# Kernel tuning notes

Hardware: AMD Instinct MI355X
Metric: run time of the kernel (lower is better)

The kernel has to match this reference:

```python
import jax, jax.numpy as jnp
import numpy as np

# Dimensions
B, V, K, H = 64, 2048, 128, 128   # graphs, verts/graph, eigenvectors, h_dim
N = B * V                          # total verts
E = 1048576                        # total neighbor entries
CF = 47                            # chem feat dim = 15 + 2*num_gdf (num_gdf=16)
L = 3                              # num_prop_layers
EPS = 1e-5                         # BatchNorm eps
PROP_SCALE = 1.0                   # propagation_time_scale


def setup_inputs() -> dict:
    key = jax.random.key(0)
    ks = iter(jax.random.split(key, 48))
    nk = lambda: next(ks)
    nrm = lambda shape, s: jax.random.normal(nk(), shape, jnp.float32) * s

    chem_feats = jax.random.normal(nk(), (E, CF), jnp.float32)
    nbr_vid = jax.random.randint(nk(), (E,), 0, N)
    # eigs layout per graph: row 0 = eigen_vals (K,), rows 1..V = eigen_vecs (V,K),
    # rows V+1..2V = eigen_vecs_inv stored as (V,K) (transposed at use site)
    eig_vals = jax.random.uniform(nk(), (B, 1, K), jnp.float32) * 2.0
    vecs = jax.random.normal(nk(), (B, V, K), jnp.float32) / np.sqrt(V)
    vecs_inv = jax.random.normal(nk(), (B, V, K), jnp.float32) / np.sqrt(V)
    eigs = jnp.concatenate([eig_vals, vecs, vecs_inv], axis=1)  # [B, 1+2V, K]

    inp = dict(chem_feats=chem_feats, nbr_vid=nbr_vid, eigs=eigs)
    # chem_mlp params
    inp.update(w1=nrm((CF, H), 0.1), b1=jnp.zeros(H), g1=jnp.ones(H), be1=jnp.zeros(H),
               w2=nrm((H, 2 * H), 0.1), b2=jnp.zeros(2 * H), g2=jnp.ones(2 * H), be2=jnp.zeros(2 * H))
    # propagation layers (stacked across L)
    inp.update(prop_time=jnp.abs(jax.random.normal(nk(), (L, H), jnp.float32)) + 0.1,
               pw1=nrm((L, 2 * H, H), 0.05), pb1=jnp.zeros((L, H)), pg1=jnp.ones((L, H)), pbe1=jnp.zeros((L, H)),
               pw2=nrm((L, H, H), 0.05), pb2=jnp.zeros((L, H)), pg2=jnp.ones((L, H)), pbe2=jnp.zeros((L, H)))
    # out_mlp params
    inp.update(wo1=nrm((H, H), 0.1), bo1=jnp.zeros(H), go1=jnp.ones(H), beo1=jnp.zeros(H),
               wo2=nrm((H, 1), 0.1), bo2=jnp.zeros(1))
    return inp


def _bn(x, g, b):
    # BatchNorm1d in training mode: biased batch stats
    m = jnp.mean(x, axis=0)
    v = jnp.var(x, axis=0)
    return g * (x - m) * jax.lax.rsqrt(v + EPS) + b


def reference(chem_feats, nbr_vid, eigs, w1, b1, g1, be1, w2, b2, g2, be2,
              prop_time, pw1, pb1, pg1, pbe1, pw2, pb2, pg2, pbe2,
              wo1, bo1, go1, beo1, wo2, bo2):
    # --- FeatExtractor ---
    h_chem = _bn(chem_feats @ w1 + b1, g1, be1)
    h_chem = jax.nn.silu(h_chem)
    h_chem = _bn(h_chem @ w2 + b2, g2, be2)             # [E, 2H]
    nbr_filter, nbr_core = h_chem[:, :H], h_chem[:, H:]
    msg = jax.nn.sigmoid(nbr_filter) * jax.nn.softplus(nbr_core)
    h = jax.ops.segment_sum(msg, nbr_vid, num_segments=N)  # [N, H]

    # --- eigen decomposition pieces (uniform per-graph sizes -> batched) ---
    eigen_vals = eigs[:, 0, :]                      # [B, K]
    evecs = eigs[:, 1:1 + V, :]                     # [B, V, K]
    evecs_inv = jnp.swapaxes(eigs[:, 1 + V:, :], 1, 2)  # [B, K, V]

    # --- PropagationLayers ---
    for l in range(L):
        pt = prop_time[l]
        # torch clamps .data in-place under no_grad, then uses it: value clamped, grad passes
        pt = pt + jax.lax.stop_gradient(jnp.clip(pt, 1e-6) - pt)
        time = PROP_SCALE * pt                      # [H]
        hb = h.reshape(B, V, H)
        h_spec = jnp.einsum('bkv,bvh->bkh', evecs_inv, hb)
        coeff = jnp.exp(-eigen_vals[:, :, None] * time[None, None, :])  # [B, K, H]
        h_prop = jnp.einsum('bvk,bkh->bvh', evecs, coeff * h_spec).reshape(N, H)
        z = jnp.concatenate([h, h_prop], axis=-1)   # [N, 2H]
        z = jax.nn.silu(_bn(z @ pw1[l] + pb1[l], pg1[l], pbe1[l]))
        z = _bn(z @ pw2[l] + pb2[l], pg2[l], pbe2[l])
        h = h + z

    # --- out_mlp + per-graph mean ---
    out = jax.nn.silu(_bn(h @ wo1 + bo1, go1, beo1)) @ wo2 + bo2  # [N, 1]
    return out.reshape(B, V, 1).mean(axis=1)        # [B, 1]
```

## Files before the change

### kernel.cpp

```cpp
#include <hip/hip_runtime.h>
#include <hip/hip_bf16.h>
#include <math.h>

#define E_N 1048576
#define CF 47
#define H 128
#define H2 256
#define B_N 64
#define V_N 2048
#define K_N 128
#define N_N 131072
#define EPSf 1e-5f
#define EVS 132

typedef __attribute__((ext_vector_type(8))) short short8;
typedef __attribute__((ext_vector_type(4))) float f32x4;

__device__ __forceinline__ float bf2f(unsigned int u16) {
  union { float f; unsigned int i; } x; x.i = u16 << 16; return x.f;
}
__device__ __forceinline__ unsigned int f2bf_rne(float f) {
  unsigned int u = __float_as_uint(f);
  return (u + 0x7fffu + ((u >> 16) & 1u)) >> 16;
}
__device__ __forceinline__ unsigned int packbf2(float lo, float hi) {
  return f2bf_rne(lo) | (f2bf_rne(hi) << 16);
}
__device__ __forceinline__ float frcp_(float x) { return __builtin_amdgcn_rcpf(x); }
__device__ __forceinline__ float sigmf_(float x) { return frcp_(1.f + __expf(-x)); }
__device__ __forceinline__ float siluf_(float x) { return x * sigmf_(x); }
__device__ __forceinline__ float splusf_(float x) {
  return (x > 15.f) ? x : __logf(1.f + __expf(x));
}

extern "C" __global__ void k_packB1(const float* __restrict__ w1, __hip_bfloat16* __restrict__ B1)
{
  const int i = blockIdx.x * 256 + threadIdx.x;
  const int j = i & 7, L = (i >> 3) & 63, s = (i >> 9) & 1, t = i >> 10;
  const int k = s * 32 + ((L >> 4) * 8) + j;
  const int n = t * 16 + (L & 15);
  B1[i] = __float2bfloat16((k < CF) ? w1[k * H + n] : 0.f);
}

extern "C" __global__ __launch_bounds__(256) void k_gemm1_stats(
    const float* __restrict__ chem, const __hip_bfloat16* __restrict__ B1,
    const float* __restrict__ b1, __hip_bfloat16* __restrict__ x1,
    float* __restrict__ sum1, float* __restrict__ ssq1)
{
  __shared__ __align__(16) unsigned short As[128 * 136];
  __shared__ float bsh[128], cs[128], cq[128];
  float* Afp = (float*)As;
  const int tid = threadIdx.x;
  const int w = tid >> 6, L = tid & 63, lm = L & 15, q = L >> 4;
  const int m0 = w * 32;
  const size_t rowbase = (size_t)blockIdx.x * 128;
  if (tid < 128) { bsh[tid] = b1[tid]; cs[tid] = 0.f; cq[tid] = 0.f; }
  for (int i = tid * 4; i < 128 * CF; i += 1024)
    *(float4*)&Afp[i] = *(const float4*)&chem[rowbase * CF + i];
  __syncthreads();

  short8 fa[2][2];
  #pragma unroll
  for (int mi = 0; mi < 2; ++mi) {
    const int row = m0 + mi * 16 + lm;
    #pragma unroll
    for (int s = 0; s < 2; ++s) {
      union { unsigned int u[4]; short8 s8; } cvt;
      #pragma unroll
      for (int jp = 0; jp < 4; ++jp) {
        const int k0i = s * 32 + q * 8 + jp * 2;
        const float lo = (k0i     < CF) ? Afp[row * CF + k0i]     : 0.f;
        const float hi = (k0i + 1 < CF) ? Afp[row * CF + k0i + 1] : 0.f;
        cvt.u[jp] = packbf2(lo, hi);
      }
      fa[mi][s] = cvt.s8;
    }
  }
  __syncthreads();

  f32x4 acc[2][8];
  #pragma unroll
  for (int mi = 0; mi < 2; ++mi)
    #pragma unroll
    for (int t = 0; t < 8; ++t) acc[mi][t] = (f32x4){0.f, 0.f, 0.f, 0.f};
  const short8* bp = (const short8*)B1;
  #pragma unroll
  for (int s = 0; s < 2; ++s)
    #pragma unroll
    for (int t = 0; t < 8; ++t) {
      const short8 bf = bp[(t * 2 + s) * 64 + L];
      acc[0][t] = __builtin_amdgcn_mfma_f32_16x16x32_bf16(fa[0][s], bf, acc[0][t], 0, 0, 0);
      acc[1][t] = __builtin_amdgcn_mfma_f32_16x16x32_bf16(fa[1][s], bf, acc[1][t], 0, 0, 0);
    }

  float cs8[8], cq8[8];
  #pragma unroll
  for (int t = 0; t < 8; ++t) { cs8[t] = 0.f; cq8[t] = 0.f; }
  #pragma unroll
  for (int t = 0; t < 8; ++t) {
    const int c = t * 16 + lm;
    const float bb = bsh[c];
    #pragma unroll
    for (int mi = 0; mi < 2; ++mi)
      #pragma unroll
      for (int r = 0; r < 4; ++r) {
        const float v = acc[mi][t][r] + bb;
        cs8[t] += v; cq8[t] += v * v;
        As[(m0 + mi * 16 + q * 4 + r) * 136 + c] = (unsigned short)f2bf_rne(v);
      }
  }
  #pragma unroll
  for (int t = 0; t < 8; ++t) {
    cs8[t] += __shfl_xor(cs8[t], 16); cs8[t] += __shfl_xor(cs8[t], 32);
    cq8[t] += __shfl_xor(cq8[t], 16); cq8[t] += __shfl_xor(cq8[t], 32);
  }
  if (q == 0) {
    #pragma unroll
    for (int t = 0; t < 8; ++t) {
      atomicAdd(&cs[t * 16 + lm], cs8[t]);
      atomicAdd(&cq[t * 16 + lm], cq8[t]);
    }
  }
  __syncthreads();
  for (int i = tid; i < 128 * 16; i += 256) {
    const int r = i >> 4, cc = (i & 15) * 8;
    *(uint4*)(x1 + (rowbase + r) * H + cc) = *(const uint4*)&As[r * 136 + cc];
  }
  if (tid < 128) {
    atomicAdd(&sum1[tid], cs[tid]);
    atomicAdd(&ssq1[tid], cq[tid]);
  }
}

extern "C" __global__ void k_bnfin(const float* __restrict__ sum, const float* __restrict__ ssq,
    const float* __restrict__ g, const float* __restrict__ be, float invn,
    float* __restrict__ sc, float* __restrict__ sh)
{
  const int c = threadIdx.x;
  const float m = sum[c] * invn;
  const float v = ssq[c] * invn - m * m;
  const float s = g[c] * rsqrtf(v + EPSf);
  sc[c] = s;
  sh[c] = be[c] - m * s;
}

extern "C" __global__ __launch_bounds__(256) void k_a1_gram(
    __hip_bfloat16* __restrict__ x1, const float* __restrict__ sc1,
    const float* __restrict__ sh1, float* __restrict__ asum, float* __restrict__ G)
{
  __shared__ __align__(16) unsigned short frag[2][16384];
  const int tid = threadIdx.x;
  const int rb = tid >> 4, u = tid & 15;
  const int kb = rb >> 2, qw = rb & 3;
  const int th = u >> 1;
  const int cmb = (u & 1) * 8;
  const int cg = u * 8;
  const int w = tid >> 6;
  const int lq = (tid >> 4) & 3;
  const int cm = tid & 15;
  const int tib = (w >> 1) * 4, tjb = (w & 1) * 4;

  float scv[8], shv[8];
  #pragma unroll
  for (int jc = 0; jc < 8; ++jc) { scv[jc] = sc1[cg + jc]; shv[jc] = sh1[cg + jc]; }

  float cs8[8] = {0.f, 0.f, 0.f, 0.f, 0.f, 0.f, 0.f, 0.f};
  f32x4 acc[4][4];
  #pragma unroll
  for (int a = 0; a < 4; ++a)
    #pragma unroll
    for (int b = 0; b < 4; ++b) acc[a][b] = (f32x4){0.f, 0.f, 0.f, 0.f};

  const int ldsbase = kb * 4096 + th * 512 + qw * 128;
  uint4 rv[8];

  auto PROCESS = [&](int bsel, size_t tb) {
    unsigned int colw[8][4];
    #pragma unroll
    for (int jc = 0; jc < 8; ++jc) { colw[jc][0] = 0; colw[jc][1] = 0; colw[jc][2] = 0; colw[jc][3] = 0; }
    #pragma unroll
    for (int j8 = 0; j8 < 8; ++j8) {
      const uint4 pk = rv[j8];
      float f[8];
      f[0] = bf2f(pk.x & 0xffff); f[1] = bf2f(pk.x >> 16);
      f[2] = bf2f(pk.y & 0xffff); f[3] = bf2f(pk.y >> 16);
      f[4] = bf2f(pk.z & 0xffff); f[5] = bf2f(pk.z >> 16);
      f[6] = bf2f(pk.w & 0xffff); f[7] = bf2f(pk.w >> 16);
      unsigned int bfv[8];
      #pragma unroll
      for (int jc = 0; jc < 8; ++jc) {
        f[jc] = siluf_(f[jc] * scv[jc] + shv[jc]);
        cs8[jc] += f[jc];
        bfv[jc] = f2bf_rne(f[jc]);
        colw[jc][j8 >> 1] |= bfv[jc] << (16 * (j8 & 1));
      }
      uint4 o;
      o.x = bfv[0] | (bfv[1] << 16); o.y = bfv[2] | (bfv[3] << 16);
      o.z = bfv[4] | (bfv[5] << 16); o.w = bfv[6] | (bfv[7] << 16);
      *(uint4*)(x1 + (tb + (size_t)(rb * 8 + j8)) * H + cg) = o;
    }
    #pragma unroll
    for (int jc = 0; jc < 8; ++jc) {
      const int pos = (cmb + jc + 2 * th) & 15;
      uint4 cw;
      cw.x = colw[jc][0]; cw.y = colw[jc][1]; cw.z = colw[jc][2]; cw.w = colw[jc][3];
      *(uint4*)&frag[bsel][ldsbase + pos * 8] = cw;
    }
  };

  {
    const size_t tb = (size_t)blockIdx.x * 128;
    #pragma unroll
    for (int j8 = 0; j8 < 8; ++j8)
      rv[j8] = *(const uint4*)(x1 + (tb + (size_t)(rb * 8 + j8)) * H + cg);
    PROCESS(0, tb);
  }

  for (int k = 0; k < 16; ++k) {
    __syncthreads();
    const int cur = k & 1;
    const bool hasnext = (k + 1 < 16);
    const size_t tbn = (size_t)(blockIdx.x + (k + 1) * 512) * 128;
    if (hasnext) {
      #pragma unroll
      for (int j8 = 0; j8 < 8; ++j8)
        rv[j8] = *(const uint4*)(x1 + (tbn + (size_t)(rb * 8 + j8)) * H + cg);
    }
    #pragma unroll
    for (int kk = 0; kk < 4; ++kk) {
      short8 fa[4], fb[4];
      #pragma unroll
      for (int a = 0; a < 4; ++a) {
        const int T = tib + a;
        fa[a] = *(const short8*)&frag[cur][kk * 4096 + T * 512 + lq * 128 + ((cm + 2 * T) & 15) * 8];
      }
      #pragma unroll
      for (int b = 0; b < 4; ++b) {
        const int T = tjb + b;
        fb[b] = *(const short8*)&frag[cur][kk * 4096 + T * 512 + lq * 128 + ((cm + 2 * T) & 15) * 8];
      }
      #pragma unroll
      for (int a = 0; a < 4; ++a)
        #pragma unroll
        for (int b = 0; b < 4; ++b)
          acc[a][b] = __builtin_amdgcn_mfma_f32_16x16x32_bf16(fa[a], fb[b], acc[a][b], 0, 0, 0);
    }
    if (hasnext) PROCESS(cur ^ 1, tbn);
  }

  #pragma unroll
  for (int jc = 0; jc < 8; ++jc) {
    cs8[jc] += __shfl_xor(cs8[jc], 16);
    cs8[jc] += __shfl_xor(cs8[jc], 32);
  }
  __syncthreads();
  float* redp = (float*)&frag[0][0];
  if ((tid & 63) < 16) {
    #pragma unroll
    for (int jc = 0; jc < 8; ++jc) redp[w * 128 + (tid & 15) * 8 + jc] = cs8[jc];
  }
  __syncthreads();
  if (tid < 128)
    atomicAdd(&asum[tid], redp[tid] + redp[128 + tid] + redp[256 + tid] + redp[384 + tid]);

  #pragma unroll
  for (int a = 0; a < 4; ++a)
    #pragma unroll
    for (int b = 0; b < 4; ++b)
      #pragma unroll
      for (int r = 0; r < 4; ++r)
        atomicAdd(&G[((tib + a) * 16 + lq * 4 + r) * 128 + (tjb + b) * 16 + cm], acc[a][b][r]);
}

extern "C" __global__ __launch_bounds__(256) void k_bn2fin(
    const float* __restrict__ asum, const float* __restrict__ Gm,
    const float* __restrict__ w2, const float* __restrict__ g2,
    const float* __restrict__ be2, float* __restrict__ sc2, float* __restrict__ sh2)
{
  __shared__ float Gs[128 * 128];
  __shared__ float w2s[128 * 128];
  __shared__ float mus[128];
  __shared__ float red[512];
  const int tid = threadIdx.x;
  const int jbase = blockIdx.x * 128;
  for (int i = tid; i < 128 * 128; i += 256) {
    Gs[i] = Gm[i];
    w2s[i] = w2[(i >> 7) * H2 + jbase + (i & 127)];
  }
  if (tid < 128) mus[tid] = asum[tid] * (1.f / (float)E_N);
  __syncthreads();
  const int jj = tid & 127, ih = tid >> 7;
  float m1 = 0.f, q = 0.f;
  for (int i = ih * 64; i < ih * 64 + 64; ++i) {
    const float wi = w2s[i * 128 + jj];
    m1 += mus[i] * wi;
    float si = 0.f;
    #pragma unroll 4
    for (int k = 0; k < 128; ++k) si += Gs[i * 128 + k] * w2s[k * 128 + jj];
    q += wi * si;
  }
  red[tid] = m1; red[256 + tid] = q;
  __syncthreads();
  if (ih == 0) {
    const float m1t = red[jj] + red[jj + 128];
    const float qt  = red[256 + jj] + red[256 + jj + 128];
    const float var = qt * (1.f / (float)E_N) - m1t * m1t;
    const float s = g2[jbase + jj] * rsqrtf(var + EPSf);
    sc2[jbase + jj] = s;
    sh2[jbase + jj] = be2[jbase + jj] - m1t * s;
  }
}

extern "C" __global__ __launch_bounds__(256) void k_hist(
    const int* __restrict__ nbr, int* __restrict__ cnt)
{
  const int e = blockIdx.x * 256 + threadIdx.x;
  atomicAdd(&cnt[nbr[e]], 1);
}

extern "C" __global__ __launch_bounds__(256) void k_scan1(
    const int* __restrict__ cnt, int* __restrict__ bsum)
{
  __shared__ int rs[256];
  const int tid = threadIdx.x, b = blockIdx.x;
  const int4 c = *(const int4*)&cnt[b * 1024 + tid * 4];
  rs[tid] = c.x + c.y + c.z + c.w;
  __syncthreads();
  for (int o = 128; o > 0; o >>= 1) {
    if (tid < o) rs[tid] += rs[tid + o];
    __syncthreads();
  }
  if (tid == 0) bsum[b] = rs[0];
}

extern "C" __global__ void k_scan2(const int* __restrict__ bsum, int* __restrict__ bpre)
{
  __shared__ int bs[128];
  const int tid = threadIdx.x;
  bs[tid] = bsum[tid];
  __syncthreads();
  int p = 0;
  for (int i = 0; i < tid; ++i) p += bs[i];
  bpre[tid] = p;
}

extern "C" __global__ __launch_bounds__(256) void k_scan3(
    const int* __restrict__ cnt, const int* __restrict__ bpre,
    int* __restrict__ cursor, int* __restrict__ rowptr)
{
  __shared__ int tsum[256];
  const int tid = threadIdx.x, b = blockIdx.x;
  const int4 c = *(const int4*)&cnt[b * 1024 + tid * 4];
  const int t1 = c.x, t2 = c.x + c.y, t3 = c.x + c.y + c.z, tot = t3 + c.w;
  tsum[tid] = tot;
  __syncthreads();
  for (int o = 1; o < 256; o <<= 1) {
    const int add = (tid >= o) ? tsum[tid - o] : 0;
    __syncthreads();
    tsum[tid] += add;
    __syncthreads();
  }
  const int excl = (tid == 0) ? 0 : tsum[tid - 1];
  const int base = bpre[b] + excl;
  int4 o4;
  o4.x = base; o4.y = base + t1; o4.z = base + t2; o4.w = base + t3;
  *(int4*)&cursor[b * 1024 + tid * 4] = o4;
  *(int4*)&rowptr[b * 1024 + tid * 4] = o4;
}

extern "C" __global__ __launch_bounds__(256) void k_scatteridx(
    const int* __restrict__ nbr, int* __restrict__ cursor,
    int* __restrict__ sorted_eid)
{
  const int e = blockIdx.x * 256 + threadIdx.x;
  const int v = nbr[e];
  const int pos = atomicAdd(&cursor[v], 1);
  sorted_eid[pos] = e;
}

extern "C" __global__ void k_packB(const float* __restrict__ w2, __hip_bfloat16* __restrict__ Bpack)
{
  const int i = blockIdx.x * 256 + threadIdx.x;
  const int j = i & 7, L = (i >> 3) & 63, s = (i >> 9) & 3, t = i >> 11;
  const int k = s * 32 + (L >> 4) * 8 + j;
  const int n = t * 16 + (L & 15);
  Bpack[i] = __float2bfloat16(w2[k * H2 + n]);
}

extern "C" __global__ __launch_bounds__(256) void k_msg(
    const __hip_bfloat16* __restrict__ a1, const int* __restrict__ sorted_eid,
    const __hip_bfloat16* __restrict__ Bpack,
    const float* __restrict__ sc2, const float* __restrict__ sh2,
    __hip_bfloat16* __restrict__ msgbuf, const int eoff)
{
  __shared__ __hip_bfloat16 As[128 * 136];
  __shared__ int eidsh[128];
  __shared__ float sc2s[256], sh2s[256];
  const int tid = threadIdx.x;
  const int s0 = blockIdx.x * 128;
  if (tid < 128) eidsh[tid] = sorted_eid[eoff + s0 + tid];
  sc2s[tid] = sc2[tid]; sh2s[tid] = sh2[tid];
  __syncthreads();
  for (int i = tid; i < 128 * 16; i += 256) {
    const int r = i >> 4, cc = (i & 15) * 8;
    *(uint4*)&As[r * 136 + cc] = *(const uint4*)(a1 + (size_t)eidsh[r] * H + cc);
  }
  __syncthreads();
  const int w = tid >> 6, L = tid & 63, lm = L & 15, q = L >> 4;
  const int m0 = w * 32, m1 = w * 32 + 16;
  f32x4 acc0[16], acc1[16];
  #pragma unroll
  for (int t = 0; t < 16; ++t) { acc0[t] = (f32x4){0.f,0.f,0.f,0.f}; acc1[t] = (f32x4){0.f,0.f,0.f,0.f}; }
  const short8* bp = (const short8*)Bpack;
  #pragma unroll
  for (int s = 0; s < 4; ++s) {
    const short8 af0 = *(const short8*)&As[(m0 + lm) * 136 + s * 32 + q * 8];
    const short8 af1 = *(const short8*)&As[(m1 + lm) * 136 + s * 32 + q * 8];
    #pragma unroll
    for (int t = 0; t < 16; ++t) {
      const short8 bf = bp[(t * 4 + s) * 64 + L];
      acc0[t] = __builtin_amdgcn_mfma_f32_16x16x32_bf16(af0, bf, acc0[t], 0, 0, 0);
      acc1[t] = __builtin_amdgcn_mfma_f32_16x16x32_bf16(af1, bf, acc1[t], 0, 0, 0);
    }
  }
  #pragma unroll
  for (int t = 0; t < 8; ++t) {
    const int cF = t * 16 + lm;
    const float scF = sc2s[cF], shF = sh2s[cF];
    const float scC = sc2s[128 + cF], shC = sh2s[128 + cF];
    #pragma unroll
    for (int r = 0; r < 4; ++r) {
      const int row0 = m0 + q * 4 + r, row1 = m1 + q * 4 + r;
      const float f0 = acc0[t][r] * scF + shF;
      const float g0 = acc0[t + 8][r] * scC + shC;
      const float f1 = acc1[t][r] * scF + shF;
      const float g1 = acc1[t + 8][r] * scC + shC;
      ((unsigned short*)As)[row0 * 136 + cF] = (unsigned short)f2bf_rne(sigmf_(f0) * splusf_(g0));
      ((unsigned short*)As)[row1 * 136 + cF] = (unsigned short)f2bf_rne(sigmf_(f1) * splusf_(g1));
    }
  }
  __syncthreads();
  for (int i = tid; i < 128 * 16; i += 256) {
    const int r = i >> 4, cc = (i & 15) * 8;
    *(uint4*)(msgbuf + ((size_t)(s0 + r)) * H + cc) = *(const uint4*)&As[r * 136 + cc];
  }
}

extern "C" __global__ __launch_bounds__(256) void k_segsum(
    const __hip_bfloat16* __restrict__ msgbuf, const int* __restrict__ rowptr,
    const int* __restrict__ cnt, float* __restrict__ h,
    const int w0, const int w1, const int mode)
{
  __shared__ float redA[256], redB[256];
  const int tid = threadIdx.x;
  const int c2 = (tid & 63) * 2;
  const int j  = tid >> 6;
  const int n0 = blockIdx.x * 16;
  for (int g = 0; g < 16; ++g) {
    const int n = n0 + g;
    const int s = rowptr[n], e = s + cnt[n];
    const int lo = max(s, w0), hi = min(e, w1);
    float s0 = 0.f, s1 = 0.f;
    for (int r = lo + j; r < hi; r += 4) {
      const unsigned int pk = *(const unsigned int*)(msgbuf + ((size_t)(r - w0)) * H + c2);
      s0 += bf2f(pk & 0xffff);
      s1 += bf2f(pk >> 16);
    }
    redA[tid] = s0; redB[tid] = s1;
    __syncthreads();
    if (j == 0) {
      const int t = tid;
      const float t0 = redA[t] + redA[t + 64] + redA[t + 128] + redA[t + 192];
      const float t1 = redB[t] + redB[t + 64] + redB[t + 128] + redB[t + 192];
      float* hp = h + (size_t)n * H + c2;
      if (mode == 0) { hp[0] = t0; hp[1] = t1; }
      else           { hp[0] += t0; hp[1] += t1; }
    }
    __syncthreads();
  }
}

extern "C" __global__ __launch_bounds__(256) void k_spec(
    const float* __restrict__ eigs, const float* __restrict__ h,
    const float* __restrict__ prop_time, int l, float* __restrict__ CS)
{
  __shared__ float Ash[64 * 32];
  __shared__ float Hsh[64 * 128];
  const int tid = threadIdx.x;
  const int b = blockIdx.x >> 2;
  const int kbase = (blockIdx.x & 3) * 32;
  const int k0 = (tid >> 5) * 4;
  const int c0 = (tid & 31) * 4;
  const size_t ebase = (size_t)b * (4097 * 128);
  float acc[4][4] = {};
  for (int vb = 0; vb < V_N; vb += 64) {
    __syncthreads();
    for (int i = tid * 4; i < 64 * 32; i += 1024) {
      const int vv = i >> 5, kk = i & 31;
      *(float4*)&Ash[i] = *(const float4*)&eigs[ebase + (size_t)(2049 + vb + vv) * 128 + kbase + kk];
    }
    for (int i = tid * 4; i < 64 * 128; i += 1024)
      *(float4*)&Hsh[i] = *(const float4*)&h[((size_t)b * V_N + vb) * 128 + i];
    __syncthreads();
    for (int vv = 0; vv < 64; ++vv) {
      const float4 av = *(const float4*)&Ash[vv * 32 + k0];
      const float4 hv = *(const float4*)&Hsh[vv * 128 + c0];
      const float aa[4] = {av.x, av.y, av.z, av.w};
      const float hh[4] = {hv.x, hv.y, hv.z, hv.w};
      #pragma unroll
      for (int a = 0; a < 4; ++a)
        #pragma unroll
        for (int j = 0; j < 4; ++j) acc[a][j] += aa[a] * hh[j];
    }
  }
  #pragma unroll
  for (int a = 0; a < 4; ++a) {
    const float ev = eigs[ebase + kbase + k0 + a];
    #pragma unroll
    for (int j = 0; j < 4; ++j) {
      const float tm = fmaxf(prop_time[l * H + c0 + j], 1e-6f);
      CS[((size_t)b * K_N + kbase + k0 + a) * H + c0 + j] = __expf(-ev * tm) * acc[a][j];
    }
  }
}

extern "C" __global__ __launch_bounds__(256) void k_hprop(
    const float* __restrict__ eigs, const float* __restrict__ CS,
    float* __restrict__ hprop)
{
  __shared__ float EvT[32 * EVS];
  __shared__ float CSsh[32 * 128];
  const int tid = threadIdx.x;
  const int b = blockIdx.x >> 4;
  const int vbase = (blockIdx.x & 15) * 128;
  const int v0 = (tid >> 4) * 8;
  const int c0 = (tid & 15) * 8;
  const size_t ebase = (size_t)b * (4097 * 128);
  float acc[8][8] = {};
  for (int kb = 0; kb < K_N; kb += 32) {
    __syncthreads();
    for (int i = tid; i < 128 * 32; i += 256) {
      const int vv = i >> 5, kk = i & 31;
      EvT[kk * EVS + vv] = eigs[ebase + (size_t)(1 + vbase + vv) * 128 + kb + kk];
    }
    for (int i = tid * 4; i < 32 * 128; i += 1024)
      *(float4*)&CSsh[i] = *(const float4*)&CS[((size_t)b * K_N + kb) * 128 + i];
    __syncthreads();
    for (int kk = 0; kk < 32; ++kk) {
      const float4 ea = *(const float4*)&EvT[kk * EVS + v0];
      const float4 eb = *(const float4*)&EvT[kk * EVS + v0 + 4];
      const float4 ca = *(const float4*)&CSsh[kk * 128 + c0];
      const float4 cb = *(const float4*)&CSsh[kk * 128 + c0 + 4];
      const float ee[8] = {ea.x, ea.y, ea.z, ea.w, eb.x, eb.y, eb.z, eb.w};
      const float cc[8] = {ca.x, ca.y, ca.z, ca.w, cb.x, cb.y, cb.z, cb.w};
      #pragma unroll
      for (int a = 0; a < 8; ++a)
        #pragma unroll
        for (int j = 0; j < 8; ++j) acc[a][j] += ee[a] * cc[j];
    }
  }
  #pragma unroll
  for (int a = 0; a < 8; ++a) {
    const size_t row = ((size_t)b * V_N + vbase + v0 + a) * H;
    #pragma unroll
    for (int j = 0; j < 8; j += 4) {
      float4 o;
      o.x = acc[a][j]; o.y = acc[a][j+1]; o.z = acc[a][j+2]; o.w = acc[a][j+3];
      *(float4*)&hprop[row + c0 + j] = o;
    }
  }
}

extern "C" __global__ __launch_bounds__(256) void k_gemm(
    const float* __restrict__ A0, const float* __restrict__ A1,
    const float* __restrict__ W, const float* __restrict__ bias,
    const float* __restrict__ preSc, const float* __restrict__ preSh,
    const int preop, const int KcA, float* __restrict__ out,
    float* __restrict__ sum, float* __restrict__ ssq)
{
  __shared__ float AT[32 * EVS];
  __shared__ float Ws[32 * 128];
  __shared__ float cs[128], cq[128];
  const int tid = threadIdx.x;
  const int rbase = blockIdx.x * 128;
  const int r0 = (tid >> 4) * 8;
  const int c0 = (tid & 15) * 8;
  float acc[8][8] = {};
  for (int kb = 0; kb < KcA; kb += 32) {
    const float* Asrc = (kb < 128) ? A0 : A1;
    const int kloc = kb & 127;
    __syncthreads();
    for (int i = tid; i < 128 * 32; i += 256) {
      const int rr = i >> 5, kk = i & 31;
      float v = Asrc[((size_t)rbase + rr) * H + kloc + kk];
      if (preop) {
        v = v * preSc[kloc + kk] + preSh[kloc + kk];
        v = siluf_(v);
      }
      AT[kk * EVS + rr] = v;
    }
    for (int i = tid * 4; i < 32 * 128; i += 1024)
      *(float4*)&Ws[i] = *(const float4*)&W[(size_t)kb * 128 + i];
    __syncthreads();
    for (int kk = 0; kk < 32; ++kk) {
      const float4 aa4 = *(const float4*)&AT[kk * EVS + r0];
      const float4 ab4 = *(const float4*)&AT[kk * EVS + r0 + 4];
      const float4 wa4 = *(const float4*)&Ws[kk * 128 + c0];
      const float4 wb4 = *(const float4*)&Ws[kk * 128 + c0 + 4];
      const float ar[8] = {aa4.x, aa4.y, aa4.z, aa4.w, ab4.x, ab4.y, ab4.z, ab4.w};
      const float wr[8] = {wa4.x, wa4.y, wa4.z, wa4.w, wb4.x, wb4.y, wb4.z, wb4.w};
      #pragma unroll
      for (int a = 0; a < 8; ++a)
        #pragma unroll
        for (int j = 0; j < 8; ++j) acc[a][j] += ar[a] * wr[j];
    }
  }
  if (tid < 128) { cs[tid] = 0.f; cq[tid] = 0.f; }
  __syncthreads();
  float s8[8] = {}, q8[8] = {};
  #pragma unroll
  for (int a = 0; a < 8; ++a) {
    const size_t row = ((size_t)rbase + r0 + a) * H;
    float val[8];
    #pragma unroll
    for (int j = 0; j < 8; ++j) {
      val[j] = acc[a][j] + bias[c0 + j];
      s8[j] += val[j];
      q8[j] += val[j] * val[j];
    }
    #pragma unroll
    for (int j = 0; j < 8; j += 4) {
      float4 o; o.x = val[j]; o.y = val[j+1]; o.z = val[j+2]; o.w = val[j+3];
      *(float4*)&out[row + c0 + j] = o;
    }
  }
  #pragma unroll
  for (int j = 0; j < 8; ++j) {
    atomicAdd(&cs[c0 + j], s8[j]);
    atomicAdd(&cq[c0 + j], q8[j]);
  }
  __syncthreads();
  if (tid < 128) {
    atomicAdd(&sum[tid], cs[tid]);
    atomicAdd(&ssq[tid], cq[tid]);
  }
}

extern "C" __global__ __launch_bounds__(256) void k_hupd(
    float* __restrict__ h, const float* __restrict__ tb,
    const float* __restrict__ sc, const float* __restrict__ sh)
{
  const int i4 = blockIdx.x * 256 + threadIdx.x;
  const size_t base = (size_t)i4 * 4;
  const int c = (int)(base & 127);
  float4 t = *(const float4*)&tb[base];
  float4 hh = *(const float4*)&h[base];
  hh.x += sc[c+0]*t.x + sh[c+0];
  hh.y += sc[c+1]*t.y + sh[c+1];
  hh.z += sc[c+2]*t.z + sh[c+2];
  hh.w += sc[c+3]*t.w + sh[c+3];
  *(float4*)&h[base] = hh;
}

extern "C" __global__ __launch_bounds__(256) void k_head(
    const float* __restrict__ ta, const float* __restrict__ sc,
    const float* __restrict__ sh, const float* __restrict__ wo2,
    const float* __restrict__ bo2, float* __restrict__ out)
{
  __shared__ float w2s[128], scs[128], shs[128];
  __shared__ float wred[4];
  const int tid = threadIdx.x;
  if (tid < 128) { w2s[tid] = wo2[tid]; scs[tid] = sc[tid]; shs[tid] = sh[tid]; }
  __syncthreads();
  const int b = blockIdx.x;
  const int wave = tid >> 6, lane = tid & 63;
  const int j = lane * 2;
  const float w0 = w2s[j], w1 = w2s[j+1];
  const float s0 = scs[j], s1 = scs[j+1], t0 = shs[j], t1 = shs[j+1];
  float p = 0.f;
  for (int v = wave; v < V_N; v += 4) {
    const float2 xv = *(const float2*)&ta[((size_t)b * V_N + v) * H + j];
    float x0 = xv.x * s0 + t0; x0 = siluf_(x0);
    float x1 = xv.y * s1 + t1; x1 = siluf_(x1);
    p += x0 * w0 + x1 * w1;
  }
  #pragma unroll
  for (int off = 32; off > 0; off >>= 1) p += __shfl_down(p, off);
  if (lane == 0) wred[wave] = p;
  __syncthreads();
  if (tid == 0) out[b] = (wred[0] + wred[1] + wred[2] + wred[3]) * (1.f / V_N) + bo2[0];
}

extern "C" void kernel_launch(void* const* d_in, const int* in_sizes, int n_in,
                              void* d_out, int out_size, void* d_ws, size_t ws_size,
                              hipStream_t stream) {
  (void)in_sizes; (void)n_in; (void)out_size;
  const float* chem = (const float*)d_in[0];
  const int*   nbr  = (const int*)d_in[1];
  const float* eigs = (const float*)d_in[2];
  const float* w1   = (const float*)d_in[3];
  const float* b1   = (const float*)d_in[4];
  const float* g1   = (const float*)d_in[5];
  const float* be1  = (const float*)d_in[6];
  const float* w2   = (const float*)d_in[7];
  const float* b2   = (const float*)d_in[8];  (void)b2;
  const float* g2   = (const float*)d_in[9];
  const float* be2  = (const float*)d_in[10];
  const float* prop_time = (const float*)d_in[11];
  const float* pw1  = (const float*)d_in[12];
  const float* pb1  = (const float*)d_in[13];
  const float* pg1  = (const float*)d_in[14];
  const float* pbe1 = (const float*)d_in[15];
  const float* pw2  = (const float*)d_in[16];
  const float* pb2  = (const float*)d_in[17];
  const float* pg2  = (const float*)d_in[18];
  const float* pbe2 = (const float*)d_in[19];
  const float* wo1  = (const float*)d_in[20];
  const float* bo1  = (const float*)d_in[21];
  const float* go1  = (const float*)d_in[22];
  const float* beo1 = (const float*)d_in[23];
  const float* wo2  = (const float*)d_in[24];
  const float* bo2  = (const float*)d_in[25];

  float* ws = (float*)d_ws;
  float* h     = ws;
  float* hprop = h + (size_t)N_N * H;
  float* ta    = hprop + (size_t)N_N * H;
  float* CS    = ta + (size_t)N_N * H;
  float* acc   = CS + (size_t)B_N * K_N * H;
  float* sum1 = acc,        *ssq1 = acc + 128;
  float* sc1  = acc + 256,  *sh1  = acc + 384;
  float* asum = acc + 512;
  float* G    = acc + 640;
  float* sc2  = acc + 17024, *sh2 = acc + 17280;
  float* statS = acc + 17536;
  float* scA = acc + 19456, *shA = acc + 19584;
  float* scB = acc + 19712, *shB = acc + 19840;
  __hip_bfloat16* x1 = (__hip_bfloat16*)(acc + 19968);

  char* p = (char*)x1 + (size_t)E_N * H * 2;
  int* cnt        = (int*)p;  p += (size_t)N_N * 4;
  int* cursor     = (int*)p;  p += (size_t)N_N * 4;
  int* rowptr     = (int*)p;  p += (size_t)N_N * 4;
  int* bsum       = (int*)p;  p += 512;
  int* bpre       = (int*)p;  p += 512;
  int* sorted_eid = (int*)p;  p += (size_t)E_N * 4;
  __hip_bfloat16* Bpack = (__hip_bfloat16*)p;  p += 65536;
  __hip_bfloat16* B1pack = (__hip_bfloat16*)p; p += 16384;

  const size_t req = (size_t)(p - (char*)d_ws);
  if (ws_size < req) return;

  __hip_bfloat16* msgbuf = (__hip_bfloat16*)hprop;

  hipMemsetAsync(acc, 0, 19456 * sizeof(float), stream);
  hipMemsetAsync(cnt, 0, (size_t)N_N * sizeof(int), stream);

  k_packB1<<<32, 256, 0, stream>>>(w1, B1pack);
  k_gemm1_stats<<<E_N / 128, 256, 0, stream>>>(chem, B1pack, b1, x1, sum1, ssq1);
  k_bnfin<<<1, 128, 0, stream>>>(sum1, ssq1, g1, be1, 1.f / (float)E_N, sc1, sh1);
  k_a1_gram<<<512, 256, 0, stream>>>(x1, sc1, sh1, asum, G);
  k_bn2fin<<<2, 256, 0, stream>>>(asum, G, w2, g2, be2, sc2, sh2);

  k_packB<<<128, 256, 0, stream>>>(w2, Bpack);
  k_hist<<<E_N / 256, 256, 0, stream>>>(nbr, cnt);
  k_scan1<<<128, 256, 0, stream>>>(cnt, bsum);
  k_scan2<<<1, 128, 0, stream>>>(bsum, bpre);
  k_scan3<<<128, 256, 0, stream>>>(cnt, bpre, cursor, rowptr);
  k_scatteridx<<<E_N / 256, 256, 0, stream>>>(nbr, cursor, sorted_eid);

  for (int half = 0; half < 2; ++half) {
    const int w0 = half * (E_N / 2), w1e = w0 + E_N / 2;
    k_msg<<<(E_N / 2) / 128, 256, 0, stream>>>(x1, sorted_eid, Bpack, sc2, sh2, msgbuf, w0);
    k_segsum<<<N_N / 16, 256, 0, stream>>>(msgbuf, rowptr, cnt, h, w0, w1e, half);
  }

  float* tb = hprop;
  for (int l = 0; l < 3; ++l) {
    k_spec<<<B_N * 4, 256, 0, stream>>>(eigs, h, prop_time, l, CS);
    k_hprop<<<B_N * 16, 256, 0, stream>>>(eigs, CS, hprop);
    k_gemm<<<N_N / 128, 256, 0, stream>>>(h, hprop, pw1 + (size_t)l * H2 * H, pb1 + l * H,
                                          nullptr, nullptr, 0, H2, ta,
                                          statS + (2 * l) * 256, statS + (2 * l) * 256 + 128);
    k_bnfin<<<1, 128, 0, stream>>>(statS + (2 * l) * 256, statS + (2 * l) * 256 + 128,
                                   pg1 + l * H, pbe1 + l * H, 1.f / (float)N_N, scA, shA);
    k_gemm<<<N_N / 128, 256, 0, stream>>>(ta, nullptr, pw2 + (size_t)l * H * H, pb2 + l * H,
                                          scA, shA, 1, H, tb,
                                          statS + (2 * l + 1) * 256, statS + (2 * l + 1) * 256 + 128);
    k_bnfin<<<1, 128, 0, stream>>>(statS + (2 * l + 1) * 256, statS + (2 * l + 1) * 256 + 128,
                                   pg2 + l * H, pbe2 + l * H, 1.f / (float)N_N, scB, shB);
    k_hupd<<<N_N * H / 1024, 256, 0, stream>>>(h, tb, scB, shB);
  }

  k_gemm<<<N_N / 128, 256, 0, stream>>>(h, nullptr, wo1, bo1, nullptr, nullptr, 0, H, ta,
                                        statS + 6 * 256, statS + 6 * 256 + 128);
  k_bnfin<<<1, 128, 0, stream>>>(statS + 6 * 256, statS + 6 * 256 + 128,
                                 go1, beo1, 1.f / (float)N_N, scA, shA);
  k_head<<<B_N, 256, 0, stream>>>(ta, scA, shA, wo2, bo2, (float*)d_out);
}
```

Baseline: 3.258 ms.

## Move propagation and output GEMMs to split-bf16 MFMA with prepacked weights

Replaces the scalar FP32 tiled GEMM, used for the propagation MLPs and the output MLP, with an MFMA kernel. It splits both activations and weights into bf16 hi/lo parts and accumulates three bf16 products to approximate FP32 accuracy. Weights are prepacked into the MFMA operand layout by a new pack kernel, and the BN statistics reduction is redone using wave shuffles. The goal is to cut the FP32 FMA compute cost of seven N×128 GEMMs, at the price of three times the MFMA work and a small loss of precision.

```diff
diff --git a/kernel.cpp b/kernel.cpp
--- a/kernel.cpp
+++ b/kernel.cpp
@@ -40,6 +40,20 @@
   const int k = s * 32 + ((L >> 4) * 8) + j;
   const int n = t * 16 + (L & 15);
   B1[i] = __float2bfloat16((k < CF) ? w1[k * H + n] : 0.f);
+}
+
+extern "C" __global__ void k_packW(const float* __restrict__ W,
+    __hip_bfloat16* __restrict__ hi, __hip_bfloat16* __restrict__ lo, const int NS)
+{
+  const int i = blockIdx.x * 256 + threadIdx.x;
+  const int j = i & 7, L = (i >> 3) & 63, ts = i >> 9;
+  const int s = ts % NS, t = ts / NS;
+  const int k = s * 32 + (L >> 4) * 8 + j;
+  const int n = t * 16 + (L & 15);
+  const float w = W[k * H + n];
+  const unsigned int h16 = f2bf_rne(w);
+  ((unsigned short*)hi)[i] = (unsigned short)h16;
+  ((unsigned short*)lo)[i] = (unsigned short)f2bf_rne(w - bf2f(h16));
 }
 
 extern "C" __global__ __launch_bounds__(256) void k_gemm1_stats(
@@ -571,73 +585,105 @@
   }
 }
 
-extern "C" __global__ __launch_bounds__(256) void k_gemm(
+extern "C" __global__ __launch_bounds__(256) void k_gemmM(
     const float* __restrict__ A0, const float* __restrict__ A1,
-    const float* __restrict__ W, const float* __restrict__ bias,
-    const float* __restrict__ preSc, const float* __restrict__ preSh,
-    const int preop, const int KcA, float* __restrict__ out,
-    float* __restrict__ sum, float* __restrict__ ssq)
-{
-  __shared__ float AT[32 * EVS];
-  __shared__ float Ws[32 * 128];
-  __shared__ float cs[128], cq[128];
-  const int tid = threadIdx.x;
+    const __hip_bfloat16* __restrict__ Whi, const __hip_bfloat16* __restrict__ Wlo,
+    const float* __restrict__ bias, const float* __restrict__ preSc,
+    const float* __restrict__ preSh, const int preop, const int KcA,
+    float* __restrict__ out, float* __restrict__ sum, float* __restrict__ ssq)
+{
+  __shared__ __align__(16) unsigned short Ahi[128 * 136];
+  __shared__ __align__(16) unsigned short Alo[128 * 136];
+  __shared__ float bsh[128], cs[128], cq[128];
+  const int tid = threadIdx.x;
+  const int w = tid >> 6, L = tid & 63, lm = L & 15, q = L >> 4;
+  const int m0 = w * 32;
   const int rbase = blockIdx.x * 128;
-  const int r0 = (tid >> 4) * 8;
-  const int c0 = (tid & 15) * 8;
-  float acc[8][8] = {};
-  for (int kb = 0; kb < KcA; kb += 32) {
-    const float* Asrc = (kb < 128) ? A0 : A1;
-    const int kloc = kb & 127;
-    __syncthreads();
-    for (int i = tid; i < 128 * 32; i += 256) {
-      const int rr = i >> 5, kk = i & 31;
-      float v = Asrc[((size_t)rbase + rr) * H + kloc + kk];
-      if (preop) {
-        v = v * preSc[kloc + kk] + preSh[kloc + kk];
-        v = siluf_(v);
+  const int NS = KcA >> 5;
+  if (tid < 128) { bsh[tid] = bias[tid]; cs[tid] = 0.f; cq[tid] = 0.f; }
+
+  f32x4 acc[2][8];
+  #pragma unroll
+  for (int mi = 0; mi < 2; ++mi)
+    #pragma unroll
+    for (int t = 0; t < 8; ++t) acc[mi][t] = (f32x4){0.f, 0.f, 0.f, 0.f};
+
+  const short8* bhp = (const short8*)Whi;
+  const short8* blp = (const short8*)Wlo;
+
+  for (int hf = 0; hf < (KcA >> 7); ++hf) {
+    const float* __restrict__ Asrc = (hf == 0) ? A0 : A1;
+    __syncthreads();
+    for (int i = tid * 4; i < 128 * 128; i += 1024) {
+      const int rr = i >> 7, kk = i & 127;
+      const float4 v4 = *(const float4*)&Asrc[((size_t)rbase + rr) * H + kk];
+      float v[4] = {v4.x, v4.y, v4.z, v4.w};
+      unsigned int h4[4], l4[4];
+      #pragma unroll
+      for (int e = 0; e < 4; ++e) {
+        float vv = v[e];
+        if (preop) { vv = vv * preSc[kk + e] + preSh[kk + e]; vv = siluf_(vv); }
+        h4[e] = f2bf_rne(vv);
+        l4[e] = f2bf_rne(vv - bf2f(h4[e]));
       }
-      AT[kk * EVS + rr] = v;
-    }
-    for (int i = tid * 4; i < 32 * 128; i += 1024)
-      *(float4*)&Ws[i] = *(const float4*)&W[(size_t)kb * 128 + i];
-    __syncthreads();
-    for (int kk = 0; kk < 32; ++kk) {
-      const float4 aa4 = *(const float4*)&AT[kk * EVS + r0];
-      const float4 ab4 = *(const float4*)&AT[kk * EVS + r0 + 4];
-      const float4 wa4 = *(const float4*)&Ws[kk * 128 + c0];
-      const float4 wb4 = *(const float4*)&Ws[kk * 128 + c0 + 4];
-      const float ar[8] = {aa4.x, aa4.y, aa4.z, aa4.w, ab4.x, ab4.y, ab4.z, ab4.w};
-      const float wr[8] = {wa4.x, wa4.y, wa4.z, wa4.w, wb4.x, wb4.y, wb4.z, wb4.w};
-      #pragma unroll
-      for (int a = 0; a < 8; ++a)
+      uint2 ph, pl;
+      ph.x = h4[0] | (h4[1] << 16); ph.y = h4[2] | (h4[3] << 16);
+      pl.x = l4[0] | (l4[1] << 16); pl.y = l4[2] | (l4[3] << 16);
+      *(uint2*)&Ahi[rr * 136 + kk] = ph;
+      *(uint2*)&Alo[rr * 136 + kk] = pl;
+    }
+    __syncthreads();
+    #pragma unroll
+    for (int s = 0; s < 4; ++s) {
+      short8 ah[2], al[2];
+      #pragma unroll
+      for (int mi = 0; mi < 2; ++mi) {
+        const int row = m0 + mi * 16 + lm;
+        ah[mi] = *(const short8*)&Ahi[row * 136 + s * 32 + q * 8];
+        al[mi] = *(const short8*)&Alo[row * 136 + s * 32 + q * 8];
+      }
+      #pragma unroll
+      for (int t = 0; t < 8; ++t) {
+        const int bidx = (t * NS + hf * 4 + s) * 64 + L;
+        const short8 bh = bhp[bidx];
+        const short8 bl = blp[bidx];
         #pragma unroll
-        for (int j = 0; j < 8; ++j) acc[a][j] += ar[a] * wr[j];
-    }
-  }
-  if (tid < 128) { cs[tid] = 0.f; cq[tid] = 0.f; }
-  __syncthreads();
-  float s8[8] = {}, q8[8] = {};
-  #pragma unroll
-  for (int a = 0; a < 8; ++a) {
-    const size_t row = ((size_t)rbase + r0 + a) * H;
-    float val[8];
-    #pragma unroll
-    for (int j = 0; j < 8; ++j) {
-      val[j] = acc[a][j] + bias[c0 + j];
-      s8[j] += val[j];
-      q8[j] += val[j] * val[j];
-    }
-    #pragma unroll
-    for (int j = 0; j < 8; j += 4) {
-      float4 o; o.x = val[j]; o.y = val[j+1]; o.z = val[j+2]; o.w = val[j+3];
-      *(float4*)&out[row + c0 + j] = o;
-    }
-  }
-  #pragma unroll
-  for (int j = 0; j < 8; ++j) {
-    atomicAdd(&cs[c0 + j], s8[j]);
-    atomicAdd(&cq[c0 + j], q8[j]);
+        for (int mi = 0; mi < 2; ++mi) {
+          acc[mi][t] = __builtin_amdgcn_mfma_f32_16x16x32_bf16(ah[mi], bh, acc[mi][t], 0, 0, 0);
+          acc[mi][t] = __builtin_amdgcn_mfma_f32_16x16x32_bf16(ah[mi], bl, acc[mi][t], 0, 0, 0);
+          acc[mi][t] = __builtin_amdgcn_mfma_f32_16x16x32_bf16(al[mi], bh, acc[mi][t], 0, 0, 0);
+        }
+      }
+    }
+  }
+
+  float cs8[8], cq8[8];
+  #pragma unroll
+  for (int t = 0; t < 8; ++t) { cs8[t] = 0.f; cq8[t] = 0.f; }
+  #pragma unroll
+  for (int t = 0; t < 8; ++t) {
+    const int c = t * 16 + lm;
+    const float bb = bsh[c];
+    #pragma unroll
+    for (int mi = 0; mi < 2; ++mi)
+      #pragma unroll
+      for (int r = 0; r < 4; ++r) {
+        const float v = acc[mi][t][r] + bb;
+        cs8[t] += v; cq8[t] += v * v;
+        out[((size_t)rbase + m0 + mi * 16 + q * 4 + r) * H + c] = v;
+      }
+  }
+  #pragma unroll
+  for (int t = 0; t < 8; ++t) {
+    cs8[t] += __shfl_xor(cs8[t], 16); cs8[t] += __shfl_xor(cs8[t], 32);
+    cq8[t] += __shfl_xor(cq8[t], 16); cq8[t] += __shfl_xor(cq8[t], 32);
+  }
+  if (q == 0) {
+    #pragma unroll
+    for (int t = 0; t < 8; ++t) {
+      atomicAdd(&cs[t * 16 + lm], cs8[t]);
+      atomicAdd(&cq[t * 16 + lm], cq8[t]);
+    }
   }
   __syncthreads();
   if (tid < 128) {
@@ -747,6 +793,12 @@
   int* sorted_eid = (int*)p;  p += (size_t)E_N * 4;
   __hip_bfloat16* Bpack = (__hip_bfloat16*)p;  p += 65536;
   __hip_bfloat16* B1pack = (__hip_bfloat16*)p; p += 16384;
+  __hip_bfloat16* PW1hi = (__hip_bfloat16*)p;  p += 3 * 65536;
+  __hip_bfloat16* PW1lo = (__hip_bfloat16*)p;  p += 3 * 65536;
+  __hip_bfloat16* PW2hi = (__hip_bfloat16*)p;  p += 3 * 32768;
+  __hip_bfloat16* PW2lo = (__hip_bfloat16*)p;  p += 3 * 32768;
+  __hip_bfloat16* WO1hi = (__hip_bfloat16*)p;  p += 32768;
+  __hip_bfloat16* WO1lo = (__hip_bfloat16*)p;  p += 32768;
 
   const size_t req = (size_t)(p - (char*)d_ws);
   if (ws_size < req) return;
@@ -763,6 +815,13 @@
   k_bn2fin<<<2, 256, 0, stream>>>(asum, G, w2, g2, be2, sc2, sh2);
 
   k_packB<<<128, 256, 0, stream>>>(w2, Bpack);
+  for (int l = 0; l < 3; ++l) {
+    k_packW<<<128, 256, 0, stream>>>(pw1 + (size_t)l * H2 * H, PW1hi + (size_t)l * 32768,
+                                     PW1lo + (size_t)l * 32768, 8);
+    k_packW<<<64, 256, 0, stream>>>(pw2 + (size_t)l * H * H, PW2hi + (size_t)l * 16384,
+                                    PW2lo + (size_t)l * 16384, 4);
+  }
+  k_packW<<<64, 256, 0, stream>>>(wo1, WO1hi, WO1lo, 4);
   k_hist<<<E_N / 256, 256, 0, stream>>>(nbr, cnt);
   k_scan1<<<128, 256, 0, stream>>>(cnt, bsum);
   k_scan2<<<1, 128, 0, stream>>>(bsum, bpre);
@@ -779,21 +838,24 @@
   for (int l = 0; l < 3; ++l) {
     k_spec<<<B_N * 4, 256, 0, stream>>>(eigs, h, prop_time, l, CS);
     k_hprop<<<B_N * 16, 256, 0, stream>>>(eigs, CS, hprop);
-    k_gemm<<<N_N / 128, 256, 0, stream>>>(h, hprop, pw1 + (size_t)l * H2 * H, pb1 + l * H,
-                                          nullptr, nullptr, 0, H2, ta,
-                                          statS + (2 * l) * 256, statS + (2 * l) * 256 + 128);
+    k_gemmM<<<N_N / 128, 256, 0, stream>>>(h, hprop, PW1hi + (size_t)l * 32768,
+                                           PW1lo + (size_t)l * 32768, pb1 + l * H,
+                                           nullptr, nullptr, 0, H2, ta,
+                                           statS + (2 * l) * 256, statS + (2 * l) * 256 + 128);
     k_bnfin<<<1, 128, 0, stream>>>(statS + (2 * l) * 256, statS + (2 * l) * 256 + 128,
                                    pg1 + l * H, pbe1 + l * H, 1.f / (float)N_N, scA, shA);
-    k_gemm<<<N_N / 128, 256, 0, stream>>>(ta, nullptr, pw2 + (size_t)l * H * H, pb2 + l * H,
-                                          scA, shA, 1, H, tb,
-                                          statS + (2 * l + 1) * 256, statS + (2 * l + 1) * 256 + 128);
+    k_gemmM<<<N_N / 128, 256, 0, stream>>>(ta, nullptr, PW2hi + (size_t)l * 16384,
+                                           PW2lo + (size_t)l * 16384, pb2 + l * H,
+                                           scA, shA, 1, H, tb,
+                                           statS + (2 * l + 1) * 256, statS + (2 * l + 1) * 256 + 128);
     k_bnfin<<<1, 128, 0, stream>>>(statS + (2 * l + 1) * 256, statS + (2 * l + 1) * 256 + 128,
                                    pg2 + l * H, pbe2 + l * H, 1.f / (float)N_N, scB, shB);
     k_hupd<<<N_N * H / 1024, 256, 0, stream>>>(h, tb, scB, shB);
   }
 
-  k_gemm<<<N_N / 128, 256, 0, stream>>>(h, nullptr, wo1, bo1, nullptr, nullptr, 0, H, ta,
-                                        statS + 6 * 256, statS + 6 * 256 + 128);
+  k_gemmM<<<N_N / 128, 256, 0, stream>>>(h, nullptr, WO1hi, WO1lo, bo1,
+                                         nullptr, nullptr, 0, H, ta,
+                                         statS + 6 * 256, statS + 6 * 256 + 128);
   k_bnfin<<<1, 128, 0, stream>>>(statS + 6 * 256, statS + 6 * 256 + 128,
                                  go1, beo1, 1.f / (float)N_N, scA, shA);
   k_head<<<B_N, 256, 0, stream>>>(ta, scA, shA, wo2, bo2, (float*)d_out);
```

Result: faster. 3.143 ms (-3.5%).
